# Kernel optimization log

Hardware: AMD Instinct MI355X
Metric: run time of the kernel (lower is better)

The kernel has to match this reference:

```python
import jax, jax.numpy as jnp
import numpy as np

HEADS = 4
TOPK = 3
NUM_LAYERS = 3
LN_EPS = 1e-5

B, T, L, I, H = 64, 512, 4, 4, 768
N = T + L + I
OUT = H // HEADS


def _static_edges():
    # edges that do not depend on data (python/numpy, hoisted as constants)
    src, dst = [], []
    i = np.arange(T - 1)
    src += [i, i + 1]; dst += [i + 1, i]                       # text chain (both dirs)
    ia, la = np.arange(I), np.arange(L)
    ig, lg = np.meshgrid(T + L + ia, T + la, indexing='ij')
    src += [ig.ravel(), lg.ravel()]; dst += [lg.ravel(), ig.ravel()]  # image<->label
    g1, g2 = np.meshgrid(ia, ia, indexing='ij')
    m = g1.ravel() != g2.ravel()                               # image->image, self loops stripped by GATConv
    src += [T + L + g1.ravel()[m]]; dst += [T + L + g2.ravel()[m]]
    h1, h2 = np.meshgrid(la, la, indexing='ij')
    m2 = h1.ravel() != h2.ravel()                              # label->label, no self
    src += [T + h1.ravel()[m2]]; dst += [T + h2.ravel()[m2]]
    sl = np.arange(N)                                          # self loops added by GATConv
    src += [sl]; dst += [sl]
    return np.concatenate(src).astype(np.int32), np.concatenate(dst).astype(np.int32)

_SSRC, _SDST = _static_edges()


def _cos(a, b):
    an = a / jnp.clip(jnp.linalg.norm(a, axis=-1, keepdims=True), 1e-8)
    bn = b / jnp.clip(jnp.linalg.norm(b, axis=-1, keepdims=True), 1e-8)
    return an @ bn.T


def _edges(text_feat, label_feat, image_feat):
    _, idx_l = jax.lax.top_k(_cos(text_feat, label_feat), TOPK)   # [T,k]
    _, idx_i = jax.lax.top_k(_cos(text_feat, image_feat), TOPK)   # [T,k]
    ti = jnp.repeat(jnp.arange(T, dtype=jnp.int32), TOPK)
    lbl = (T + idx_l.reshape(-1)).astype(jnp.int32)
    img = (T + L + idx_i.reshape(-1)).astype(jnp.int32)
    src = jnp.concatenate([jnp.asarray(_SSRC), ti, lbl, ti, img])
    dst = jnp.concatenate([jnp.asarray(_SDST), lbl, ti, img, ti])
    return src, dst


def _gat_residual(x, src, dst, W, a_s, a_d, bias, gamma, beta):
    # GATConv (PyG defaults): lin without bias, additive attention, LeakyReLU(0.2),
    # softmax over incoming edges per dst, concat heads, + bias. Dropout in eval mode (off).
    h = (x @ W.T).reshape(N, HEADS, OUT)
    e = jax.nn.leaky_relu((h * a_s).sum(-1)[src] + (h * a_d).sum(-1)[dst], 0.2)  # [E,heads]
    emax = jax.ops.segment_max(e, dst, num_segments=N)
    ex = jnp.exp(e - emax[dst])
    den = jax.ops.segment_sum(ex, dst, num_segments=N)
    alpha = ex / (den[dst] + 1e-16)
    agg = jax.ops.segment_sum(alpha[:, :, None] * h[src], dst, num_segments=N)
    o = jax.nn.relu(agg.reshape(N, H) + bias)
    y = o + x
    mu = y.mean(-1, keepdims=True)
    var = ((y - mu) ** 2).mean(-1, keepdims=True)
    return (y - mu) / jnp.sqrt(var + LN_EPS) * gamma + beta


def setup_inputs() -> dict:
    key = jax.random.key(0)
    ks = jax.random.split(key, 6)
    inp = {
        'text_repr': jax.random.normal(ks[0], (B, T, H), jnp.float32),
        'label_repr': jax.random.normal(ks[1], (B, L, H), jnp.float32),
        'image_repr': jax.random.normal(ks[2], (B, I, H), jnp.float32),
        'Ws': jax.random.normal(ks[3], (NUM_LAYERS, H, H), jnp.float32) * 0.02,
        'att_srcs': jax.random.normal(ks[4], (NUM_LAYERS, HEADS, OUT), jnp.float32) * 0.1,
        'att_dsts': jax.random.normal(ks[5], (NUM_LAYERS, HEADS, OUT), jnp.float32) * 0.1,
        'biases': jnp.zeros((NUM_LAYERS, H), jnp.float32),
        'gammas': jnp.ones((NUM_LAYERS, H), jnp.float32),
        'betas': jnp.zeros((NUM_LAYERS, H), jnp.float32),
    }
    return inp


def reference(text_repr, label_repr, image_repr, Ws, att_srcs, att_dsts, biases, gammas, betas):
    def per_sample(tf, lf, imf):
        src, dst = _edges(tf, lf, imf)
        x = jnp.concatenate([tf, lf, imf], axis=0)  # [N,H]
        for l in range(NUM_LAYERS):
            x = _gat_residual(x, src, dst, Ws[l], att_srcs[l], att_dsts[l],
                              biases[l], gammas[l], betas[l])
        return x[:T]
    return jax.vmap(per_sample)(text_repr, label_repr, image_repr)
```

## Files before the change

kernel.cpp:

```cpp
#include <hip/hip_runtime.h>
#include <math.h>

#define B 64
#define T 512
#define H 768
#define DOUT 192
#define MTEXT (B*T)
#define MSPEC (B*8)

typedef unsigned short u16;
typedef __attribute__((ext_vector_type(8))) short short8;
typedef __attribute__((ext_vector_type(4))) short s4v;
typedef __attribute__((ext_vector_type(4))) float floatx4;

__device__ __forceinline__ float bf2f(u16 u){
  union { float f; unsigned int i; } v; v.i = ((unsigned int)u) << 16; return v.f;
}
__device__ __forceinline__ u16 f2bf(float f){
  unsigned int u = __float_as_uint(f);
  unsigned int lsb = (u >> 16) & 1u;
  u += 0x7fffu + lsb;
  return (u16)(u >> 16);
}
__device__ __forceinline__ float lrelu(float v){ return v > 0.f ? v : 0.2f*v; }
__device__ __forceinline__ float ldv(const void* p, size_t i, int isF32){
  return isF32 ? ((const float*)p)[i] : bf2f(((const u16*)p)[i]);
}

__global__ __launch_bounds__(256) void detect_kernel(const u16* __restrict__ raw, int* __restrict__ flag){
  __shared__ int red[256];
  int tid = threadIdx.x;
  int cnt = 0;
  for (int i = tid; i < 2048; i += 256){
    u16 u = raw[(size_t)i*2];
    int e = (u >> 7) & 0xFF;
    if (e >= 110 && e <= 135) cnt++;
  }
  red[tid] = cnt; __syncthreads();
  for (int s = 128; s > 0; s >>= 1){ if (tid < s) red[tid] += red[tid+s]; __syncthreads(); }
  if (tid == 0) *flag = (red[0] < 1024) ? 1 : 0;
}

__global__ __launch_bounds__(256) void convert_kernel(const void* __restrict__ src,
                                                      u16* __restrict__ dst, int n,
                                                      const int* __restrict__ flagp){
  int i = blockIdx.x*256 + threadIdx.x;
  if (i >= n) return;
  if (*flagp) dst[i] = f2bf(((const float*)src)[i]);
  else        dst[i] = ((const u16*)src)[i];
}

__global__ __launch_bounds__(256) void convert_text_kernel(const void* __restrict__ src,
                                                           u16* __restrict__ dst,
                                                           const int* __restrict__ flagp){
  size_t i = (size_t)blockIdx.x*256 + threadIdx.x;
  if (*flagp){
    float4 v = ((const float4*)src)[i];
    s4v o;
    o[0] = (short)f2bf(v.x); o[1] = (short)f2bf(v.y);
    o[2] = (short)f2bf(v.z); o[3] = (short)f2bf(v.w);
    ((s4v*)dst)[i] = o;
  } else {
    ((s4v*)dst)[i] = ((const s4v*)src)[i];
  }
}

__global__ __launch_bounds__(256) void prep_spec_kernel(const void* __restrict__ label,
                                                        const void* __restrict__ image,
                                                        u16* __restrict__ xs,
                                                        float* __restrict__ norms2,
                                                        const int* __restrict__ flagp){
  __shared__ float red[256];
  int isF32 = *flagp;
  int rr = blockIdx.x;
  int tid = threadIdx.x;
  int b = rr >> 3, s = rr & 7;
  const void* srcb = (s < 4) ? label : image;
  size_t base = (size_t)(b*4 + (s & 3))*H;
  float sq = 0.f;
  #pragma unroll
  for (int r = 0; r < 3; r++){
    int dd = tid + r*256;
    float f = ldv(srcb, base + dd, isF32);
    xs[(size_t)rr*H + dd] = f2bf(f);
    sq += f*f;
  }
  red[tid] = sq; __syncthreads();
  for (int ss = 128; ss > 0; ss >>= 1){ if (tid < ss) red[tid] += red[tid+ss]; __syncthreads(); }
  if (tid == 0) norms2[rr] = red[0];
}

__global__ __launch_bounds__(256) void topk_kernel(const void* __restrict__ text,
                                                   const void* __restrict__ label,
                                                   const void* __restrict__ image,
                                                   const float* __restrict__ norms2,
                                                   int* __restrict__ excl_l,
                                                   int* __restrict__ excl_i,
                                                   const int* __restrict__ flagp){
  __shared__ float spec[8*H];
  int isF32 = *flagp;
  int tid = threadIdx.x, wave = tid >> 6, lane = tid & 63;
  int b = blockIdx.y;

  if (isF32){
    const float* lb = (const float*)label + (size_t)b*4*H;
    const float* im = (const float*)image + (size_t)b*4*H;
    #pragma unroll
    for (int j = 0; j < 6; j++){
      int idx = tid + j*256;
      int flat = idx*4;
      int s = flat / H, d = flat % H;
      const float* src = (s < 4) ? (lb + (size_t)s*H + d) : (im + (size_t)(s-4)*H + d);
      *(float4*)(spec + s*H + d) = *(const float4*)src;
    }
  } else {
    const u16* lb = (const u16*)label + (size_t)b*4*H;
    const u16* im = (const u16*)image + (size_t)b*4*H;
    #pragma unroll
    for (int j = 0; j < 6; j++){
      int idx = tid + j*256;
      int flat = idx*4;
      int s = flat / H, d = flat % H;
      const u16* src = (s < 4) ? (lb + (size_t)s*H + d) : (im + (size_t)(s-4)*H + d);
      s4v v = *(const s4v*)src;
      float4 f;
      f.x = bf2f((u16)v[0]); f.y = bf2f((u16)v[1]);
      f.z = bf2f((u16)v[2]); f.w = bf2f((u16)v[3]);
      *(float4*)(spec + s*H + d) = f;
    }
  }
  __syncthreads();

  #pragma unroll
  for (int pass = 0; pass < 4; pass++){
    int t = blockIdx.x*16 + pass*4 + wave;
    size_t tb = ((size_t)b*T + t)*H;
    float tx[12];
    if (isF32){
      const float* tp = (const float*)text + tb;
      #pragma unroll
      for (int k = 0; k < 3; k++){
        float4 v = *(const float4*)(tp + lane*4 + k*256);
        tx[k*4+0]=v.x; tx[k*4+1]=v.y; tx[k*4+2]=v.z; tx[k*4+3]=v.w;
      }
    } else {
      const u16* tp = (const u16*)text + tb;
      #pragma unroll
      for (int k = 0; k < 3; k++){
        s4v v = *(const s4v*)(tp + lane*4 + k*256);
        tx[k*4+0]=bf2f((u16)v[0]); tx[k*4+1]=bf2f((u16)v[1]);
        tx[k*4+2]=bf2f((u16)v[2]); tx[k*4+3]=bf2f((u16)v[3]);
      }
    }
    float dot[8] = {0,0,0,0,0,0,0,0};
    #pragma unroll
    for (int k = 0; k < 3; k++){
      int d = lane*4 + k*256;
      #pragma unroll
      for (int s = 0; s < 8; s++){
        float4 sv = *(const float4*)(spec + s*H + d);
        dot[s] += tx[k*4+0]*sv.x + tx[k*4+1]*sv.y + tx[k*4+2]*sv.z + tx[k*4+3]*sv.w;
      }
    }
    #pragma unroll
    for (int s = 0; s < 8; s++)
      for (int o = 32; o > 0; o >>= 1) dot[s] += __shfl_down(dot[s], o);
    if (lane == 0){
      float vl[4], vi[4];
      #pragma unroll
      for (int j = 0; j < 4; j++){
        vl[j] = dot[j]   / fmaxf(sqrtf(norms2[b*8 + j]),     1e-8f);
        vi[j] = dot[4+j] / fmaxf(sqrtf(norms2[b*8 + 4 + j]), 1e-8f);
      }
      int el = 0, ei = 0;
      #pragma unroll
      for (int j = 1; j < 4; j++){
        if (vl[j] <= vl[el]) el = j;
        if (vi[j] <= vi[ei]) ei = j;
      }
      excl_l[b*T + t] = el;
      excl_i[b*T + t] = ei;
    }
  }
}

__global__ __launch_bounds__(256) void gemm_kernel(const void* __restrict__ At, int arow0,
                                                   const u16* __restrict__ As,
                                                   const u16* __restrict__ Bw,
                                                   u16* __restrict__ C,
                                                   int text_tiles, int ctext,
                                                   int forceBf,
                                                   const int* __restrict__ flagp){
  __shared__ __align__(16) u16 lA[128*72];
  __shared__ __align__(16) u16 lB[128*72];
  int isF32 = forceBf ? 0 : *flagp;
  int tid = threadIdx.x;

  int nb = gridDim.x;
  int bid = blockIdx.x;
  int q = nb >> 3, r = nb & 7;
  int xcd = bid & 7, ixx = bid >> 3;
  int lid = (xcd < r ? xcd*(q+1) : r*(q+1) + (xcd - r)*q) + ixx;
  int tile = lid / 6;
  int nbase = (lid % 6) * 128;

  bool spec = (tile >= text_tiles);
  int lrow0 = spec ? (tile - text_tiles)*128 : tile*128;
  int crow0 = spec ? (ctext + lrow0) : lrow0;
  const u16*   Abf = spec ? (As + (size_t)lrow0*H)
                          : ((const u16*)At + (size_t)(arow0 + lrow0)*H);
  const float* Af  = (const float*)At + (size_t)(arow0 + lrow0)*H;
  int wave = tid >> 6, lane = tid & 63;
  int wm = (wave >> 1) * 64, wn = (wave & 1) * 64;
  int lrow = lane & 15, lkq = (lane >> 4) * 8;
  int r0 = tid >> 3;
  int c0 = (tid & 7) * 8;

  floatx4 acc[4][4];
  #pragma unroll
  for (int i = 0; i < 4; i++)
    #pragma unroll
    for (int j = 0; j < 4; j++)
      acc[i][j] = (floatx4){0.f,0.f,0.f,0.f};

  for (int k0 = 0; k0 < H; k0 += 64){
    short8 va[4], vb[4];
    #pragma unroll
    for (int i = 0; i < 4; i++){
      int row = i*32 + r0;
      if (spec || !isF32) va[i] = *(const short8*)(Abf + (size_t)row*H + k0 + c0);
      else {
        const float* p = Af + (size_t)row*H + k0 + c0;
        float4 lo = *(const float4*)p;
        float4 hi = *(const float4*)(p + 4);
        short8 tv;
        tv[0]=(short)f2bf(lo.x); tv[1]=(short)f2bf(lo.y); tv[2]=(short)f2bf(lo.z); tv[3]=(short)f2bf(lo.w);
        tv[4]=(short)f2bf(hi.x); tv[5]=(short)f2bf(hi.y); tv[6]=(short)f2bf(hi.z); tv[7]=(short)f2bf(hi.w);
        va[i] = tv;
      }
      vb[i] = *(const short8*)(Bw + (size_t)(nbase + row)*H + k0 + c0);
    }
    __syncthreads();
    #pragma unroll
    for (int i = 0; i < 4; i++){
      int row = i*32 + r0;
      *(short8*)(lA + row*72 + c0) = va[i];
      *(short8*)(lB + row*72 + c0) = vb[i];
    }
    __syncthreads();
    #pragma unroll
    for (int kk = 0; kk < 2; kk++){
      short8 af[4], bfv[4];
      #pragma unroll
      for (int i = 0; i < 4; i++){
        af[i]  = *(const short8*)(lA + (wm + i*16 + lrow)*72 + kk*32 + lkq);
        bfv[i] = *(const short8*)(lB + (wn + i*16 + lrow)*72 + kk*32 + lkq);
      }
      #pragma unroll
      for (int i = 0; i < 4; i++)
        #pragma unroll
        for (int j = 0; j < 4; j++)
          acc[i][j] = __builtin_amdgcn_mfma_f32_16x16x32_bf16(af[i], bfv[j], acc[i][j], 0, 0, 0);
    }
  }
  int qrow = (lane >> 4) * 4;
  int col = lane & 15;
  #pragma unroll
  for (int i = 0; i < 4; i++)
    #pragma unroll
    for (int j = 0; j < 4; j++)
      #pragma unroll
      for (int r2 = 0; r2 < 4; r2++){
        int grow = crow0 + wm + i*16 + qrow + r2;
        int gcol = nbase + wn + j*16 + col;
        C[(size_t)grow*H + gcol] = f2bf(acc[i][j][r2]);
      }
}

__global__ __launch_bounds__(256) void node_att_kernel(const u16* __restrict__ h,
                                                       const u16* __restrict__ a_s,
                                                       const u16* __restrict__ a_d,
                                                       float* __restrict__ es,
                                                       float* __restrict__ ed,
                                                       int nnodes){
  int tid = threadIdx.x, wave = tid >> 6, lane = tid & 63;
  int node = blockIdx.x*4 + wave;
  if (node >= nnodes) return;
  int head = lane >> 4, i16 = lane & 15;
  int off = head*DOUT + i16*12;
  const u16* hp = h + (size_t)node*H + off;
  float s = 0.f, d = 0.f;
  #pragma unroll
  for (int k = 0; k < 3; k++){
    s4v hv = *(const s4v*)(hp + k*4);
    s4v sv = *(const s4v*)(a_s + off + k*4);
    s4v dv = *(const s4v*)(a_d + off + k*4);
    #pragma unroll
    for (int c = 0; c < 4; c++){
      float hf = bf2f((u16)hv[c]);
      s += hf * bf2f((u16)sv[c]);
      d += hf * bf2f((u16)dv[c]);
    }
  }
  #pragma unroll
  for (int o = 8; o > 0; o >>= 1){ s += __shfl_down(s, o); d += __shfl_down(d, o); }
  if (i16 == 0){ es[node*4 + head] = s; ed[node*4 + head] = d; }
}

__global__ __launch_bounds__(256) void attn_text_kernel(
    const u16* __restrict__ h,
    const u16* __restrict__ xres,
    const void* __restrict__ xraw,
    int xrow0,
    void* __restrict__ xout,
    u16* __restrict__ xoutbf,
    const float* __restrict__ es, const float* __restrict__ ed,
    const int* __restrict__ exl_c, const int* __restrict__ exi_c,
    const u16* __restrict__ bias, const u16* __restrict__ gamma, const u16* __restrict__ beta,
    int ctext, int resBf, int outRaw, const int* __restrict__ flagp){
  __shared__ float alpha_l[4][9][4];

  int isF32 = *flagp;
  int tid = threadIdx.x, wave = tid >> 6, lane = tid & 63;

  int nb = gridDim.x;
  int bid = blockIdx.x;
  int q = nb >> 3, r = nb & 7;
  int xcd = bid & 7, ixx = bid >> 3;
  int lb = (xcd < r ? xcd*(q+1) : r*(q+1) + (xcd - r)*q) + ixx;

  int loc = lb*4 + wave;
  int bloc = loc >> 9, t = loc & 511;
  int el = exl_c[loc], ei = exi_c[loc];
  int sbase = ctext + bloc*8;

  int e = lane >> 2, hh = lane & 3;
  bool act = (e < 9) && !(e == 1 && t == 0) && !(e == 2 && t == T-1);
  int srcE;
  if (e == 0)      srcE = loc;
  else if (e == 1) srcE = loc - 1;
  else if (e == 2) srcE = loc + 1;
  else if (e < 6){ int k = e - 3; srcE = sbase + k + (k >= el ? 1 : 0); }
  else           { int k = e - 6; srcE = sbase + 4 + (k & 3) + ((k & 3) >= ei ? 1 : 0); }
  float v = -1e30f;
  if (act) v = lrelu(es[srcE*4 + hh] + ed[loc*4 + hh]);
  float m = v;
  #pragma unroll
  for (int o = 4; o < 64; o <<= 1) m = fmaxf(m, __shfl_xor(m, o));
  float w = act ? expf(fminf(v - m, 0.f)) : 0.f;
  float den = w;
  #pragma unroll
  for (int o = 4; o < 64; o <<= 1) den += __shfl_xor(den, o);
  if (e < 9) alpha_l[wave][e][hh] = w / (den + 1e-16f);
  __syncthreads();

  int srcs[9];
  srcs[0] = loc;
  srcs[1] = (t > 0)   ? loc - 1 : loc;
  srcs[2] = (t < T-1) ? loc + 1 : loc;
  #pragma unroll
  for (int k = 0; k < 3; k++){
    srcs[3+k] = sbase + k + (k >= el ? 1 : 0);
    srcs[6+k] = sbase + 4 + k + (k >= ei ? 1 : 0);
  }

  int d0 = lane*4;
  int hk0 = d0/DOUT, hk1 = (d0+256)/DOUT, hk2 = (d0+512)/DOUT;
  float a0[4] = {0,0,0,0}, a1[4] = {0,0,0,0}, a2[4] = {0,0,0,0};
  #pragma unroll
  for (int ee = 0; ee < 9; ee++){
    const u16* hp = h + (size_t)srcs[ee]*H + d0;
    s4v v0 = *(const s4v*)(hp);
    s4v v1 = *(const s4v*)(hp + 256);
    s4v v2 = *(const s4v*)(hp + 512);
    float al0 = alpha_l[wave][ee][hk0];
    float al1 = alpha_l[wave][ee][hk1];
    float al2 = alpha_l[wave][ee][hk2];
    #pragma unroll
    for (int c = 0; c < 4; c++){
      a0[c] += al0 * bf2f((u16)v0[c]);
      a1[c] += al1 * bf2f((u16)v1[c]);
      a2[c] += al2 * bf2f((u16)v2[c]);
    }
  }

  size_t xoff = (size_t)(xrow0 + loc)*H + d0;
  s4v b0 = *(const s4v*)(bias + d0);
  s4v b1 = *(const s4v*)(bias + d0 + 256);
  s4v b2 = *(const s4v*)(bias + d0 + 512);
  float xr0[4], xr1[4], xr2[4];
  if (resBf){
    const u16* xp = xres + xoff;
    s4v x0 = *(const s4v*)xp;
    s4v x1 = *(const s4v*)(xp + 256);
    s4v x2 = *(const s4v*)(xp + 512);
    #pragma unroll
    for (int c = 0; c < 4; c++){
      xr0[c] = bf2f((u16)x0[c]); xr1[c] = bf2f((u16)x1[c]); xr2[c] = bf2f((u16)x2[c]);
    }
  } else if (isF32){
    const float* xp = (const float*)xraw + xoff;
    float4 x0 = *(const float4*)xp;
    float4 x1 = *(const float4*)(xp + 256);
    float4 x2 = *(const float4*)(xp + 512);
    xr0[0]=x0.x; xr0[1]=x0.y; xr0[2]=x0.z; xr0[3]=x0.w;
    xr1[0]=x1.x; xr1[1]=x1.y; xr1[2]=x1.z; xr1[3]=x1.w;
    xr2[0]=x2.x; xr2[1]=x2.y; xr2[2]=x2.z; xr2[3]=x2.w;
  } else {
    const u16* xp = (const u16*)xraw + xoff;
    s4v x0 = *(const s4v*)xp;
    s4v x1 = *(const s4v*)(xp + 256);
    s4v x2 = *(const s4v*)(xp + 512);
    #pragma unroll
    for (int c = 0; c < 4; c++){
      xr0[c] = bf2f((u16)x0[c]); xr1[c] = bf2f((u16)x1[c]); xr2[c] = bf2f((u16)x2[c]);
    }
  }
  float y0[4], y1[4], y2[4];
  float sum = 0.f, sumsq = 0.f;
  #pragma unroll
  for (int c = 0; c < 4; c++){
    y0[c] = fmaxf(a0[c] + bf2f((u16)b0[c]), 0.f) + xr0[c];
    y1[c] = fmaxf(a1[c] + bf2f((u16)b1[c]), 0.f) + xr1[c];
    y2[c] = fmaxf(a2[c] + bf2f((u16)b2[c]), 0.f) + xr2[c];
    sum   += y0[c] + y1[c] + y2[c];
    sumsq += y0[c]*y0[c] + y1[c]*y1[c] + y2[c]*y2[c];
  }
  #pragma unroll
  for (int o = 1; o < 64; o <<= 1){
    sum   += __shfl_xor(sum, o);
    sumsq += __shfl_xor(sumsq, o);
  }
  float mean = sum * (1.f/H);
  float var = sumsq * (1.f/H) - mean*mean;
  float rstd = rsqrtf(fmaxf(var, 0.f) + 1e-5f);
  s4v g0 = *(const s4v*)(gamma + d0);
  s4v g1 = *(const s4v*)(gamma + d0 + 256);
  s4v g2 = *(const s4v*)(gamma + d0 + 512);
  s4v be0 = *(const s4v*)(beta + d0);
  s4v be1 = *(const s4v*)(beta + d0 + 256);
  s4v be2 = *(const s4v*)(beta + d0 + 512);
  float o0[4], o1[4], o2[4];
  #pragma unroll
  for (int c = 0; c < 4; c++){
    o0[c] = (y0[c] - mean) * rstd * bf2f((u16)g0[c]) + bf2f((u16)be0[c]);
    o1[c] = (y1[c] - mean) * rstd * bf2f((u16)g1[c]) + bf2f((u16)be1[c]);
    o2[c] = (y2[c] - mean) * rstd * bf2f((u16)g2[c]) + bf2f((u16)be2[c]);
  }
  if (!outRaw){
    u16* xo = xoutbf + xoff;
    s4v w0, w1, w2;
    #pragma unroll
    for (int c = 0; c < 4; c++){
      w0[c] = (short)f2bf(o0[c]); w1[c] = (short)f2bf(o1[c]); w2[c] = (short)f2bf(o2[c]);
    }
    *(s4v*)xo = w0; *(s4v*)(xo + 256) = w1; *(s4v*)(xo + 512) = w2;
  } else if (isF32){
    float* xo = (float*)xout + xoff;
    float4 w0, w1, w2;
    w0.x=o0[0]; w0.y=o0[1]; w0.z=o0[2]; w0.w=o0[3];
    w1.x=o1[0]; w1.y=o1[1]; w1.z=o1[2]; w1.w=o1[3];
    w2.x=o2[0]; w2.y=o2[1]; w2.z=o2[2]; w2.w=o2[3];
    *(float4*)xo = w0; *(float4*)(xo + 256) = w1; *(float4*)(xo + 512) = w2;
  } else {
    u16* xo = (u16*)xout + xoff;
    s4v w0, w1, w2;
    #pragma unroll
    for (int c = 0; c < 4; c++){
      w0[c] = (short)f2bf(o0[c]); w1[c] = (short)f2bf(o1[c]); w2[c] = (short)f2bf(o2[c]);
    }
    *(s4v*)xo = w0; *(s4v*)(xo + 256) = w1; *(s4v*)(xo + 512) = w2;
  }
}

__global__ __launch_bounds__(256) void attn_spec_kernel(
    const u16* __restrict__ h, u16* __restrict__ xs_c,
    const float* __restrict__ es, const float* __restrict__ ed,
    const int* __restrict__ exl_c, const int* __restrict__ exi_c,
    const u16* __restrict__ bias, const u16* __restrict__ gamma, const u16* __restrict__ beta,
    int ctext){
  __shared__ float wred[16];
  __shared__ float wdyn[512][4];
  __shared__ float sw[8][4];
  __shared__ float wm4[4][4], wsum4[4][4];

  int tid = threadIdx.x, wave = tid >> 6, lane = tid & 63;

  int nb = gridDim.x;
  int bid = blockIdx.x;
  int q = nb >> 3, r = nb & 7;
  int xcd = bid & 7, ixx = bid >> 3;
  int idx = (xcd < r ? xcd*(q+1) : r*(q+1) + (xcd - r)*q) + ixx;

  int bloc = idx >> 3, s = idx & 7;
  int node = ctext + idx;
  const int* excl = (s < 4) ? exl_c : exi_c;
  int target = s & 3;
  float edv[4];
  #pragma unroll
  for (int hh = 0; hh < 4; hh++) edv[hh] = ed[node*4 + hh];

  int t0 = tid, t1 = tid + 256;
  bool sel0 = (excl[bloc*512 + t0] != target);
  bool sel1 = (excl[bloc*512 + t1] != target);
  const float* e0 = es + (size_t)(bloc*512 + t0)*4;
  const float* e1 = es + (size_t)(bloc*512 + t1)*4;
  float v0[4], v1[4], vs[4], m[4];
  #pragma unroll
  for (int hh = 0; hh < 4; hh++){
    v0[hh] = sel0 ? lrelu(e0[hh] + edv[hh]) : -1e30f;
    v1[hh] = sel1 ? lrelu(e1[hh] + edv[hh]) : -1e30f;
    m[hh] = fmaxf(v0[hh], v1[hh]);
  }
  if (tid < 8){
    const float* ep = es + (size_t)(ctext + bloc*8 + tid)*4;
    #pragma unroll
    for (int hh = 0; hh < 4; hh++){ vs[hh] = lrelu(ep[hh] + edv[hh]); m[hh] = fmaxf(m[hh], vs[hh]); }
  }
  #pragma unroll
  for (int hh = 0; hh < 4; hh++)
    for (int o = 32; o > 0; o >>= 1) m[hh] = fmaxf(m[hh], __shfl_down(m[hh], o));
  if (lane == 0){
    #pragma unroll
    for (int hh = 0; hh < 4; hh++) wm4[wave][hh] = m[hh];
  }
  __syncthreads();
  #pragma unroll
  for (int hh = 0; hh < 4; hh++)
    m[hh] = fmaxf(fmaxf(wm4[0][hh], wm4[1][hh]), fmaxf(wm4[2][hh], wm4[3][hh]));

  float ds[4];
  #pragma unroll
  for (int hh = 0; hh < 4; hh++){
    float w0 = sel0 ? expf(fminf(v0[hh] - m[hh], 0.f)) : 0.f;
    float w1 = sel1 ? expf(fminf(v1[hh] - m[hh], 0.f)) : 0.f;
    wdyn[t0][hh] = w0; wdyn[t1][hh] = w1;
    ds[hh] = w0 + w1;
  }
  if (tid < 8){
    #pragma unroll
    for (int hh = 0; hh < 4; hh++){
      float w = expf(fminf(vs[hh] - m[hh], 0.f));
      sw[tid][hh] = w; ds[hh] += w;
    }
  }
  #pragma unroll
  for (int hh = 0; hh < 4; hh++)
    for (int o = 32; o > 0; o >>= 1) ds[hh] += __shfl_down(ds[hh], o);
  if (lane == 0){
    #pragma unroll
    for (int hh = 0; hh < 4; hh++) wsum4[wave][hh] = ds[hh];
  }
  __syncthreads();

  int cc = tid;
  int hh4 = (cc < 192) ? (cc/48) : 0;
  float dinv = 1.f / (wsum4[0][hh4] + wsum4[1][hh4] + wsum4[2][hh4] + wsum4[3][hh4] + 1e-16f);
  float agg[4] = {0.f, 0.f, 0.f, 0.f};
  if (cc < 192){
    const u16* hp = h + (size_t)(bloc*512)*H + cc*4;
    #pragma unroll 8
    for (int tt = 0; tt < 512; tt++){
      s4v hv = *(const s4v*)(hp + (size_t)tt*H);
      float wv = wdyn[tt][hh4];
      agg[0] += wv * bf2f((u16)hv[0]);
      agg[1] += wv * bf2f((u16)hv[1]);
      agg[2] += wv * bf2f((u16)hv[2]);
      agg[3] += wv * bf2f((u16)hv[3]);
    }
    #pragma unroll
    for (int e2 = 0; e2 < 8; e2++){
      s4v hv = *(const s4v*)(h + (size_t)(ctext + bloc*8 + e2)*H + cc*4);
      float wv = sw[e2][hh4];
      agg[0] += wv * bf2f((u16)hv[0]);
      agg[1] += wv * bf2f((u16)hv[1]);
      agg[2] += wv * bf2f((u16)hv[2]);
      agg[3] += wv * bf2f((u16)hv[3]);
    }
  }
  float y[4] = {0.f,0.f,0.f,0.f};
  float sum = 0.f, sumsq = 0.f;
  if (cc < 192){
    s4v bv = *(const s4v*)(bias + cc*4);
    s4v xv = *(const s4v*)(xs_c + (size_t)idx*H + cc*4);
    #pragma unroll
    for (int c = 0; c < 4; c++){
      float a = agg[c] * dinv;
      float o = fmaxf(a + bf2f((u16)bv[c]), 0.f);
      float yv = o + bf2f((u16)xv[c]);
      y[c] = yv; sum += yv; sumsq += yv*yv;
    }
  }
  for (int o = 32; o > 0; o >>= 1){ sum += __shfl_down(sum, o); sumsq += __shfl_down(sumsq, o); }
  if (lane == 0){ wred[wave] = sum; wred[8 + wave] = sumsq; }
  __syncthreads();
  sum   = wred[0] + wred[1] + wred[2] + wred[3];
  sumsq = wred[8] + wred[9] + wred[10] + wred[11];
  float mean = sum * (1.f/H);
  float var = sumsq * (1.f/H) - mean*mean;
  float rstd = rsqrtf(fmaxf(var, 0.f) + 1e-5f);
  if (cc < 192){
    s4v gv = *(const s4v*)(gamma + cc*4);
    s4v bev = *(const s4v*)(beta + cc*4);
    s4v wv;
    #pragma unroll
    for (int c = 0; c < 4; c++){
      float o = (y[c] - mean) * rstd * bf2f((u16)gv[c]) + bf2f((u16)bev[c]);
      wv[c] = (short)f2bf(o);
    }
    *(s4v*)(xs_c + (size_t)idx*H + cc*4) = wv;
  }
}

extern "C" void kernel_launch(void* const* d_in, const int* in_sizes, int n_in,
                              void* d_out, int out_size, void* d_ws, size_t ws_size,
                              hipStream_t stream){
  const void* text  = d_in[0];
  const void* label = d_in[1];
  const void* image = d_in[2];

  auto align256 = [](size_t x){ return (x + 255) & ~(size_t)255; };
  auto baseNeed = [&](int cand) -> size_t {
    int ct = MTEXT/cand, cs = MSPEC/cand;
    int st = (cs + 127)/128;
    size_t hr = (size_t)ct + (size_t)st*128;
    return align256(4)
         + align256(hr*H*2)
         + align256((size_t)(MSPEC+64)*H*2)
         + 2*align256((size_t)MTEXT*4)
         + align256((size_t)MSPEC*4)
         + 2*align256(hr*4*4)
         + align256((size_t)3*H*H*2)
         + 5*align256((size_t)3*H*2);
  };
  size_t bfExtra = 2*align256((size_t)MTEXT*H*2);

  int useBf = 0, nch = 8;
  for (int cand = 1; cand <= 8; cand <<= 1){
    if (baseNeed(cand) + bfExtra <= ws_size){ useBf = 1; nch = cand; break; }
  }
  if (!useBf){
    for (int cand = 1; cand <= 8; cand <<= 1){
      if (baseNeed(cand) <= ws_size || cand == 8){ nch = cand; break; }
    }
  }
  int ctext = MTEXT/nch, cspec = MSPEC/nch;
  int spec_tiles = (cspec + 127)/128;
  int hrows = ctext + spec_tiles*128;
  int text_tiles = ctext / 128;

  char* ws = (char*)d_ws;
  size_t off = 0;
  auto alloc = [&](size_t bytes) -> void* {
    void* p = ws + off; off += (bytes + 255) & ~(size_t)255; return p;
  };
  int*   flag = (int*)  alloc(4);
  u16*   h    = (u16*)  alloc((size_t)hrows*H*2);
  u16*   xs   = (u16*)  alloc((size_t)(MSPEC+64)*H*2);
  int*   exl  = (int*)  alloc((size_t)MTEXT*4);
  int*   exi  = (int*)  alloc((size_t)MTEXT*4);
  float* nrm  = (float*)alloc((size_t)MSPEC*4);
  float* es   = (float*)alloc((size_t)hrows*4*4);
  float* ed   = (float*)alloc((size_t)hrows*4*4);
  u16*   Wc   = (u16*)  alloc((size_t)3*H*H*2);
  u16*   asc  = (u16*)  alloc((size_t)3*H*2);
  u16*   adc  = (u16*)  alloc((size_t)3*H*2);
  u16*   bc   = (u16*)  alloc((size_t)3*H*2);
  u16*   gc   = (u16*)  alloc((size_t)3*H*2);
  u16*   bec  = (u16*)  alloc((size_t)3*H*2);
  u16*   xt_bf = nullptr;
  u16*   xint  = nullptr;
  if (useBf){
    xt_bf = (u16*)alloc((size_t)MTEXT*H*2);
    xint  = (u16*)alloc((size_t)MTEXT*H*2);
  }

  detect_kernel<<<1, 256, 0, stream>>>((const u16*)text, flag);
  convert_kernel<<<(3*H*H + 255)/256, 256, 0, stream>>>(d_in[3], Wc, 3*H*H, flag);
  convert_kernel<<<9, 256, 0, stream>>>(d_in[4], asc, 3*H, flag);
  convert_kernel<<<9, 256, 0, stream>>>(d_in[5], adc, 3*H, flag);
  convert_kernel<<<9, 256, 0, stream>>>(d_in[6], bc,  3*H, flag);
  convert_kernel<<<9, 256, 0, stream>>>(d_in[7], gc,  3*H, flag);
  convert_kernel<<<9, 256, 0, stream>>>(d_in[8], bec, 3*H, flag);

  prep_spec_kernel<<<MSPEC, 256, 0, stream>>>(label, image, xs, nrm, flag);
  topk_kernel<<<dim3(T/16, B), 256, 0, stream>>>(text, label, image, nrm, exl, exi, flag);
  if (useBf)
    convert_text_kernel<<<(MTEXT*H/4 + 255)/256, 256, 0, stream>>>(text, xt_bf, flag);

  for (int l = 0; l < 3; l++){
    const void* At; int forceBf;
    if (useBf){ At = (l == 0) ? (const void*)xt_bf : (const void*)xint; forceBf = 1; }
    else      { At = (l == 0) ? text : (const void*)d_out;              forceBf = 0; }
    const u16* xres = useBf ? ((l == 0) ? xt_bf : xint) : nullptr;
    const void* xraw = (l == 0) ? text : (const void*)d_out;
    int outRaw = (!useBf) || (l == 2);

    for (int c = 0; c < nch; c++){
      gemm_kernel<<<(text_tiles + spec_tiles)*6, 256, 0, stream>>>(
          At, c*ctext, xs + (size_t)c*cspec*H, Wc + (size_t)l*H*H, h,
          text_tiles, ctext, forceBf, flag);
      node_att_kernel<<<(ctext + cspec + 3)/4, 256, 0, stream>>>(
          h, asc + l*H, adc + l*H, es, ed, ctext + cspec);
      attn_spec_kernel<<<cspec, 256, 0, stream>>>(
          h, xs + (size_t)c*cspec*H, es, ed,
          exl + c*ctext, exi + c*ctext,
          bc + l*H, gc + l*H, bec + l*H, ctext);
      attn_text_kernel<<<ctext/4, 256, 0, stream>>>(
          h, xres, xraw, c*ctext, d_out, xint,
          es, ed, exl + c*ctext, exi + c*ctext,
          bc + l*H, gc + l*H, bec + l*H,
          ctext, useBf, outRaw, flag);
    }
  }
}
```

Baseline: 669.3 us.

## Fuse per-node attention score dot products into GEMM epilogue with atomics

Removes the separate node_att kernel. The GEMM epilogue now dots its fp32 accumulators with att_src/att_dst, reduces across 16 lanes with shuffles, and atomically adds partial per-head scores into es/ed. A zeroing kernel clears es/ed before each GEMM. This avoids re-reading h from memory and one launch per chunk, at the cost of atomics and extra epilogue work. Scores are now computed from fp32 accumulators rather than bf16-rounded h, so results differ slightly.

Measured after the change: 848.3 us. 26.7% more time.

```diff
diff --git a/kernel.cpp b/kernel.cpp
--- a/kernel.cpp
+++ b/kernel.cpp
@@ -39,6 +39,11 @@
   red[tid] = cnt; __syncthreads();
   for (int s = 128; s > 0; s >>= 1){ if (tid < s) red[tid] += red[tid+s]; __syncthreads(); }
   if (tid == 0) *flag = (red[0] < 1024) ? 1 : 0;
+}
+
+__global__ __launch_bounds__(256) void zero2_kernel(float* __restrict__ a, float* __restrict__ b, int n){
+  int i = blockIdx.x*256 + threadIdx.x;
+  if (i < n){ a[i] = 0.f; b[i] = 0.f; }
 }
 
 __global__ __launch_bounds__(256) void convert_kernel(const void* __restrict__ src,
@@ -188,6 +193,10 @@
                                                    const u16* __restrict__ As,
                                                    const u16* __restrict__ Bw,
                                                    u16* __restrict__ C,
+                                                   const u16* __restrict__ asc_g,
+                                                   const u16* __restrict__ adc_g,
+                                                   float* __restrict__ es,
+                                                   float* __restrict__ ed,
                                                    int text_tiles, int ctext,
                                                    int forceBf,
                                                    const int* __restrict__ flagp){
@@ -275,36 +284,37 @@
         int gcol = nbase + wn + j*16 + col;
         C[(size_t)grow*H + gcol] = f2bf(acc[i][j][r2]);
       }
-}
-
-__global__ __launch_bounds__(256) void node_att_kernel(const u16* __restrict__ h,
-                                                       const u16* __restrict__ a_s,
-                                                       const u16* __restrict__ a_d,
-                                                       float* __restrict__ es,
-                                                       float* __restrict__ ed,
-                                                       int nnodes){
-  int tid = threadIdx.x, wave = tid >> 6, lane = tid & 63;
-  int node = blockIdx.x*4 + wave;
-  if (node >= nnodes) return;
-  int head = lane >> 4, i16 = lane & 15;
-  int off = head*DOUT + i16*12;
-  const u16* hp = h + (size_t)node*H + off;
-  float s = 0.f, d = 0.f;
-  #pragma unroll
-  for (int k = 0; k < 3; k++){
-    s4v hv = *(const s4v*)(hp + k*4);
-    s4v sv = *(const s4v*)(a_s + off + k*4);
-    s4v dv = *(const s4v*)(a_d + off + k*4);
-    #pragma unroll
-    for (int c = 0; c < 4; c++){
-      float hf = bf2f((u16)hv[c]);
-      s += hf * bf2f((u16)sv[c]);
-      d += hf * bf2f((u16)dv[c]);
-    }
-  }
-  #pragma unroll
-  for (int o = 8; o > 0; o >>= 1){ s += __shfl_down(s, o); d += __shfl_down(d, o); }
-  if (i16 == 0){ es[node*4 + head] = s; ed[node*4 + head] = d; }
+
+  int headw = (nbase + wn) / DOUT;
+  float as4[4], ad4[4];
+  #pragma unroll
+  for (int j = 0; j < 4; j++){
+    int gc2 = nbase + wn + j*16 + col;
+    as4[j] = bf2f(asc_g[gc2]);
+    ad4[j] = bf2f(adc_g[gc2]);
+  }
+  #pragma unroll
+  for (int i = 0; i < 4; i++)
+    #pragma unroll
+    for (int r2 = 0; r2 < 4; r2++){
+      float sv = 0.f, dv = 0.f;
+      #pragma unroll
+      for (int j = 0; j < 4; j++){
+        float v = acc[i][j][r2];
+        sv += v * as4[j];
+        dv += v * ad4[j];
+      }
+      #pragma unroll
+      for (int o = 8; o > 0; o >>= 1){
+        sv += __shfl_down(sv, o, 16);
+        dv += __shfl_down(dv, o, 16);
+      }
+      if (col == 0){
+        int grow = crow0 + wm + i*16 + qrow + r2;
+        atomicAdd(&es[(size_t)grow*4 + headw], sv);
+        atomicAdd(&ed[(size_t)grow*4 + headw], dv);
+      }
+    }
 }
 
 __global__ __launch_bounds__(256) void attn_text_kernel(
@@ -697,11 +707,11 @@
     int outRaw = (!useBf) || (l == 2);
 
     for (int c = 0; c < nch; c++){
+      zero2_kernel<<<(hrows*4 + 255)/256, 256, 0, stream>>>(es, ed, hrows*4);
       gemm_kernel<<<(text_tiles + spec_tiles)*6, 256, 0, stream>>>(
           At, c*ctext, xs + (size_t)c*cspec*H, Wc + (size_t)l*H*H, h,
+          asc + l*H, adc + l*H, es, ed,
           text_tiles, ctext, forceBf, flag);
-      node_att_kernel<<<(ctext + cspec + 3)/4, 256, 0, stream>>>(
-          h, asc + l*H, adc + l*H, es, ed, ctext + cspec);
       attn_spec_kernel<<<cspec, 256, 0, stream>>>(
           h, xs + (size_t)c*cspec*H, es, ed,
           exl + c*ctext, exi + c*ctext,
```
